# Kernel tuning notes

Hardware: AMD Instinct MI355X
Metric: run time of the kernel (lower is better)

The kernel has to match this reference:

```python
import jax, jax.numpy as jnp
import numpy as np

B, N, K, D, H = 16384, 10, 5, 512, 2
HD = D // H  # 256
IMG = 512.0


def setup_inputs() -> dict:
    key = jax.random.key(0)
    ks = jax.random.split(key, 18)
    w = lambda k, shape: (jax.random.normal(k, shape) * 0.02).astype(jnp.float32)
    boxes = jax.random.uniform(ks[0], (B, N, 4), minval=0.0, maxval=IMG, dtype=jnp.float32)
    return {
        'boxes': boxes,
        'w_in': w(ks[1], (D, K * 4)), 'b_in': jnp.zeros((D,), jnp.float32),
        'wqkv': w(ks[2], (3 * D, D)), 'bqkv': jnp.zeros((3 * D,), jnp.float32),
        'wo': w(ks[3], (D, D)), 'bo': jnp.zeros((D,), jnp.float32),
        'ln1_w': jnp.ones((D,), jnp.float32), 'ln1_b': jnp.zeros((D,), jnp.float32),
        'w1': w(ks[4], (D, D)), 'b1': jnp.zeros((D,), jnp.float32),
        'w2': w(ks[5], (D, D)), 'b2': jnp.zeros((D,), jnp.float32),
        'ln2_w': jnp.ones((D,), jnp.float32), 'ln2_b': jnp.zeros((D,), jnp.float32),
        'lnf_w': jnp.ones((D,), jnp.float32), 'lnf_b': jnp.zeros((D,), jnp.float32),
    }


def _ln(x, w, b, eps=1e-5):
    mu = jnp.mean(x, -1, keepdims=True)
    var = jnp.mean((x - mu) ** 2, -1, keepdims=True)
    return (x - mu) * jax.lax.rsqrt(var + eps) * w + b


def _relationships(boxes):
    # boxes: [B, N, 4] -> rel: [B, N, K*4]
    cx = (boxes[..., 0] + boxes[..., 2]) * 0.5 / IMG
    cy = (boxes[..., 1] + boxes[..., 3]) * 0.5 / IMG
    bw = jnp.abs(boxes[..., 2] - boxes[..., 0]) / IMG
    bh = jnp.abs(boxes[..., 3] - boxes[..., 1]) / IMG
    feats = jnp.stack([cx, cy, bw, bh], -1)  # [B, N, 4]
    dx = cx[:, :, None] - cx[:, None, :]
    dy = cy[:, :, None] - cy[:, None, :]
    dists = dx * dx + dy * dy  # [B, N, N]
    dists = jnp.where(jnp.eye(N, dtype=bool), jnp.inf, dists)
    _, idx = jax.lax.top_k(-dists, K)  # K smallest, ascending -> [B, N, K]
    nbr = jnp.take_along_axis(jnp.broadcast_to(feats[:, None], (B, N, N, 4)), idx[:, :, :, None], axis=2)  # [B, N, K, 4]
    return (nbr - feats[:, :, None, :]).reshape(B, N, K * 4)


def reference(boxes, w_in, b_in, wqkv, bqkv, wo, bo, ln1_w, ln1_b, w1, b1, w2, b2, ln2_w, ln2_b, lnf_w, lnf_b):
    rel = _relationships(boxes)                      # [B, N, 20]
    x = rel @ w_in.T + b_in                          # [B, N, D]
    # --- self attention (post-norm TransformerEncoderLayer, eval mode: no dropout) ---
    qkv = x @ wqkv.T + bqkv
    q, k, v = jnp.split(qkv, 3, axis=-1)
    split_heads = lambda t: t.reshape(B, N, H, HD).transpose(0, 2, 1, 3)
    q, k, v = split_heads(q), split_heads(k), split_heads(v)
    scores = jnp.einsum('bhqd,bhkd->bhqk', q, k) / jnp.sqrt(jnp.float32(HD))
    att = jax.nn.softmax(scores, axis=-1)
    o = jnp.einsum('bhqk,bhkd->bhqd', att, v).transpose(0, 2, 1, 3).reshape(B, N, D)
    x = _ln(x + o @ wo.T + bo, ln1_w, ln1_b)
    # --- feed forward ---
    ff = jax.nn.gelu(x @ w1.T + b1, approximate=False) @ w2.T + b2
    x = _ln(x + ff, ln2_w, ln2_b)
    return _ln(x, lnf_w, lnf_b)
```

## Files before the change

kernel.cpp:

```cpp
#include <hip/hip_runtime.h>
#include <hip/hip_bf16.h>
#include <math.h>

#define B_   16384
#define NT   10
#define KNN  5
#define D_   512
#define MTOT (B_*NT)

typedef __bf16 bf;
typedef __bf16 bfrag8 __attribute__((ext_vector_type(8)));
typedef float  floatx4 __attribute__((ext_vector_type(4)));

__device__ __forceinline__ float tof(bf x) { return (float)x; }
__device__ __forceinline__ bf    tob(float x) { return (bf)x; }

#define GLD_LDS(g, l) __builtin_amdgcn_global_load_lds( \
    (const __attribute__((address_space(1))) void*)(g), \
    (__attribute__((address_space(3))) void*)(l), 16, 0, 0)

__global__ void prep_folds(const float* __restrict__ wqkv, const float* __restrict__ bqkv,
                           const float* __restrict__ wo,   const float* __restrict__ bo,
                           bf* __restrict__ At, bf* __restrict__ Ct,
                           float* __restrict__ wconst, float* __restrict__ uvec)
{
    int gid = blockIdx.x, tid = threadIdx.x;
    if (gid < 4096) {
        int idx = gid * 256 + tid;
        int mat = idx >> 18;
        int rem = idx & 262143;
        int row = rem >> 9, col = rem & 511;
        float acc = 0.f;
        if (mat < 2) {
            int h = mat;
            const float* wq = wqkv + (size_t)(h * 256) * 512;
            const float* wk = wqkv + (size_t)(512 + h * 256) * 512;
            for (int c = 0; c < 256; ++c)
                acc += wq[c * 512 + col] * wk[c * 512 + row];
            At[(size_t)h * 262144 + row * 512 + col] = tob(acc * 0.0625f);
        } else {
            int h = mat - 2;
            const float* wv = wqkv + (size_t)(1024 + h * 256) * 512;
            for (int e = 0; e < 256; ++e)
                acc += wv[e * 512 + col] * wo[row * 512 + h * 256 + e];
            Ct[(size_t)h * 262144 + row * 512 + col] = tob(acc);
        }
    } else {
        for (int d = tid; d < 512; d += 256) {
            float acc = bo[d];
            for (int e = 0; e < 512; ++e)
                acc += bqkv[1024 + e] * wo[d * 512 + e];
            wconst[d] = acc;
            for (int h = 0; h < 2; ++h) {
                float u = 0.f;
                for (int c = 0; c < 256; ++c)
                    u += wqkv[(size_t)(512 + h * 256 + c) * 512 + d] * bqkv[h * 256 + c];
                uvec[h * 512 + d] = u * 0.0625f;
            }
        }
    }
}

__global__ void cvt_w(const float* __restrict__ src, bf* __restrict__ dst)
{
    int i = blockIdx.x * 256 + threadIdx.x;
    float4 v = *(const float4*)(src + (size_t)i * 4);
    bf o[4] = { tob(v.x), tob(v.y), tob(v.z), tob(v.w) };
    *(unsigned long long*)(dst + (size_t)i * 4) = *(unsigned long long*)o;
}

__global__ void rel_kernel(const float* __restrict__ boxes, float* __restrict__ rel)
{
#pragma clang fp contract(off)
    int gid = blockIdx.x * blockDim.x + threadIdx.x;
    if (gid >= MTOT) return;
    int b = gid / NT, n = gid % NT;
    const float* bx = boxes + (size_t)b * NT * 4;
    float cx[NT], cy[NT], bw[NT], bh[NT];
#pragma unroll
    for (int j = 0; j < NT; ++j) {
        float x0 = bx[j * 4 + 0], y0 = bx[j * 4 + 1];
        float x1 = bx[j * 4 + 2], y1 = bx[j * 4 + 3];
        cx[j] = ((x0 + x1) * 0.5f) * (1.f / 512.f);
        cy[j] = ((y0 + y1) * 0.5f) * (1.f / 512.f);
        bw[j] = fabsf(x1 - x0) * (1.f / 512.f);
        bh[j] = fabsf(y1 - y0) * (1.f / 512.f);
    }
    float dist[NT];
#pragma unroll
    for (int j = 0; j < NT; ++j) {
        float dx = cx[n] - cx[j], dy = cy[n] - cy[j];
        float dxx = dx * dx, dyy = dy * dy;
        dist[j] = (j == n) ? __builtin_inff() : (dxx + dyy);
    }
    float ocx = cx[n], ocy = cy[n], obw = bw[n], obh = bh[n];
#pragma unroll
    for (int k = 0; k < KNN; ++k) {
        int best = 0; float bd = __builtin_inff();
#pragma unroll
        for (int j = 0; j < NT; ++j)
            if (dist[j] < bd) { bd = dist[j]; best = j; }
        float fx = 0, fy = 0, fw = 0, fh = 0;
#pragma unroll
        for (int j = 0; j < NT; ++j)
            if (j == best) { fx = cx[j]; fy = cy[j]; fw = bw[j]; fh = bh[j]; dist[j] = __builtin_inff(); }
        size_t o = (size_t)gid * 20 + k * 4;
        rel[o + 0] = fx - ocx;
        rel[o + 1] = fy - ocy;
        rel[o + 2] = fw - obw;
        rel[o + 3] = fh - obh;
    }
}

__global__ void gemm_in(const float* __restrict__ rel, const float* __restrict__ w_in,
                        const float* __restrict__ b_in, bf* __restrict__ x0)
{
    __shared__ float relS[128][20];
    int tid = threadIdx.x;
    size_t tok0 = (size_t)blockIdx.x * 128;
    for (int i = tid; i < 128 * 20; i += 256)
        relS[i / 20][i % 20] = rel[tok0 * 20 + i];
    float w0[20], w1r[20];
#pragma unroll
    for (int j = 0; j < 20; ++j) {
        w0[j]  = w_in[tid * 20 + j];
        w1r[j] = w_in[(tid + 256) * 20 + j];
    }
    float bias0 = b_in[tid], bias1 = b_in[tid + 256];
    __syncthreads();
    for (int tk = 0; tk < 128; ++tk) {
        float a0 = bias0, a1 = bias1;
#pragma unroll
        for (int j = 0; j < 20; ++j) {
            float r = relS[tk][j];
            a0 += r * w0[j];
            a1 += r * w1r[j];
        }
        x0[(tok0 + tk) * 512 + tid]       = tob(a0);
        x0[(tok0 + tk) * 512 + tid + 256] = tob(a1);
    }
}

template <int EPI>
__launch_bounds__(512, 2)
__global__ void gemm_fn(const bf* __restrict__ A, const bf* __restrict__ Bt,
                        bf* __restrict__ out, const float* __restrict__ biasf)
{
    __shared__ bf As[2][128 * 32];
    __shared__ bf Bs[2][512 * 32];
    int tid = threadIdx.x;
    int w = tid >> 6, l = tid & 63;
    int lq = l >> 4, lr = l & 15;
    size_t m0 = (size_t)blockIdx.x * 128;
    int wm = (w & 1) * 64, wn = (w >> 1) * 128;
    floatx4 acc[4][8] = {};

    const bf* Ag = A + (m0 + (tid & 127)) * 512 + (tid >> 7) * 8;
    const bf* Bg = Bt + (size_t)tid * 512;

    auto stage = [&](int buf, int kt) {
        GLD_LDS(Ag + kt * 32, &As[buf][w * 512]);
#pragma unroll
        for (int p = 0; p < 4; ++p)
            GLD_LDS(Bg + kt * 32 + p * 8, &Bs[buf][(p * 512 + w * 64) * 8]);
    };

    stage(0, 0);
    asm volatile("s_waitcnt vmcnt(0)" ::: "memory");
    __builtin_amdgcn_s_barrier();
    __builtin_amdgcn_sched_barrier(0);

#pragma unroll 2
    for (int kt = 0; kt < 16; ++kt) {
        int cur = kt & 1;
        if (kt < 15) stage(cur ^ 1, kt + 1);

        const bf* as = &As[cur][(lq * 128 + wm + lr) * 8];
        const bf* bs = &Bs[cur][(lq * 512 + wn + lr) * 8];
        bfrag8 af[4], bfv[8];
#pragma unroll
        for (int i = 0; i < 4; ++i)
            af[i] = *(const bfrag8*)(as + i * 16 * 8);
#pragma unroll
        for (int j = 0; j < 8; ++j)
            bfv[j] = *(const bfrag8*)(bs + j * 16 * 8);
#pragma unroll
        for (int i = 0; i < 4; ++i)
#pragma unroll
            for (int j = 0; j < 8; ++j)
                acc[i][j] = __builtin_amdgcn_mfma_f32_16x16x32_bf16(af[i], bfv[j], acc[i][j], 0, 0, 0);

        if (kt < 15) {
            asm volatile("s_waitcnt vmcnt(0) lgkmcnt(0)" ::: "memory");
            __builtin_amdgcn_s_barrier();
            __builtin_amdgcn_sched_barrier(0);
        }
    }

#pragma unroll
    for (int i = 0; i < 4; ++i)
#pragma unroll
        for (int j = 0; j < 8; ++j) {
            int col = wn + j * 16 + lr;
#pragma unroll
            for (int r = 0; r < 4; ++r) {
                int row = wm + i * 16 + lq * 4 + r;
                float v = acc[i][j][r];
                if (EPI == 1) { v += biasf[col]; v = 0.5f * v * (1.f + erff(v * 0.70710678118654752f)); }
                if (EPI == 2) v += biasf[col];
                if (EPI == 3) v += tof(out[(m0 + row) * 512 + col]);
                out[(m0 + row) * 512 + col] = tob(v);
            }
        }
}

__global__ void scores_kernel(const bf* __restrict__ t, const bf* __restrict__ x0,
                              const float* __restrict__ uvec_h, float* __restrict__ att)
{
    int tid = threadIdx.x;
    int w = tid >> 6, l = tid & 63;
    int lq = l >> 4, lr = l & 15;
    size_t b = (size_t)blockIdx.x * 4 + w;
    const bf* trow = t  + (b * NT + lr) * 512;
    const bf* xrow = x0 + (b * NT + lr) * 512;
    floatx4 acc = {0.f, 0.f, 0.f, 0.f};
    float xu = 0.f;
#pragma unroll
    for (int kk = 0; kk < 16; ++kk) {
        bfrag8 a  = *(const bfrag8*)(trow + kk * 32 + lq * 8);
        bfrag8 bb = *(const bfrag8*)(xrow + kk * 32 + lq * 8);
        acc = __builtin_amdgcn_mfma_f32_16x16x32_bf16(a, bb, acc, 0, 0, 0);
#pragma unroll
        for (int jj = 0; jj < 8; ++jj)
            xu += (float)bb[jj] * uvec_h[kk * 32 + lq * 8 + jj];
    }
    xu += __shfl_xor(xu, 16);
    xu += __shfl_xor(xu, 32);
    bool jvalid = (lr < NT);
    float* ab = att + b * 100;
#pragma unroll
    for (int r = 0; r < 4; ++r) {
        float v = jvalid ? (acc[r] + xu) : -__builtin_inff();
        float m = v;
        m = fmaxf(m, __shfl_xor(m, 1)); m = fmaxf(m, __shfl_xor(m, 2));
        m = fmaxf(m, __shfl_xor(m, 4)); m = fmaxf(m, __shfl_xor(m, 8));
        float e = jvalid ? __expf(v - m) : 0.f;
        float s = e;
        s += __shfl_xor(s, 1); s += __shfl_xor(s, 2);
        s += __shfl_xor(s, 4); s += __shfl_xor(s, 8);
        float a = e / s;
        int i = lq * 4 + r;
        if (jvalid && i < NT) ab[i * 10 + lr] = a;
    }
}

__global__ void zmix(const float* __restrict__ att, const bf* __restrict__ x0, bf* __restrict__ z)
{
    __shared__ float xs[NT][512];
    __shared__ float as[100];
    size_t b = blockIdx.x;
    int tid = threadIdx.x;
    const bf* xb = x0 + b * NT * 512;
    for (int i = tid; i < NT * 512; i += 256) xs[i >> 9][i & 511] = tof(xb[i]);
    for (int i = tid; i < 100; i += 256) as[i] = att[b * 100 + i];
    __syncthreads();
    bf* zb = z + b * NT * 512;
    for (int o = tid; o < NT * 512; o += 256) {
        int i = o >> 9, d = o & 511;
        float a = 0.f;
#pragma unroll
        for (int j = 0; j < NT; ++j) a += as[i * 10 + j] * xs[j][d];
        zb[o] = tob(a);
    }
}

__global__ void ln_kernel(const bf* __restrict__ xin, const bf* __restrict__ yin,
                          const float* __restrict__ w, const float* __restrict__ bias,
                          bf* __restrict__ xout)
{
    int tid = threadIdx.x;
    int wv = tid >> 6, l = tid & 63;
    size_t tok = (size_t)blockIdx.x * 4 + wv;
    bfrag8 xv = *(const bfrag8*)(xin + tok * 512 + l * 8);
    bfrag8 yv = *(const bfrag8*)(yin + tok * 512 + l * 8);
    float v[8]; float s = 0.f;
#pragma unroll
    for (int i = 0; i < 8; ++i) { v[i] = (float)xv[i] + (float)yv[i]; s += v[i]; }
#pragma unroll
    for (int m = 1; m < 64; m <<= 1) s += __shfl_xor(s, m);
    float mu = s * (1.f / 512.f);
    float vs = 0.f;
#pragma unroll
    for (int i = 0; i < 8; ++i) { float d = v[i] - mu; vs += d * d; }
#pragma unroll
    for (int m = 1; m < 64; m <<= 1) vs += __shfl_xor(vs, m);
    float r = rsqrtf(vs * (1.f / 512.f) + 1e-5f);
    bfrag8 ov;
#pragma unroll
    for (int i = 0; i < 8; ++i) {
        int d = l * 8 + i;
        ov[i] = tob((v[i] - mu) * r * w[d] + bias[d]);
    }
    *(bfrag8*)(xout + tok * 512 + l * 8) = ov;
}

__global__ void final_kernel(const bf* __restrict__ x1, const bf* __restrict__ ff2,
                             const float* __restrict__ w2, const float* __restrict__ b2,
                             const float* __restrict__ wf, const float* __restrict__ bfi,
                             float* __restrict__ out)
{
    int tid = threadIdx.x;
    int wv = tid >> 6, l = tid & 63;
    size_t tok = (size_t)blockIdx.x * 4 + wv;
    bfrag8 xv = *(const bfrag8*)(x1 + tok * 512 + l * 8);
    bfrag8 yv = *(const bfrag8*)(ff2 + tok * 512 + l * 8);
    float v[8]; float s = 0.f;
#pragma unroll
    for (int i = 0; i < 8; ++i) { v[i] = (float)xv[i] + (float)yv[i]; s += v[i]; }
#pragma unroll
    for (int m = 1; m < 64; m <<= 1) s += __shfl_xor(s, m);
    float mu = s * (1.f / 512.f);
    float vs = 0.f;
#pragma unroll
    for (int i = 0; i < 8; ++i) { float d = v[i] - mu; vs += d * d; }
#pragma unroll
    for (int m = 1; m < 64; m <<= 1) vs += __shfl_xor(vs, m);
    float r = rsqrtf(vs * (1.f / 512.f) + 1e-5f);
    float u[8]; float s2 = 0.f;
#pragma unroll
    for (int i = 0; i < 8; ++i) {
        int d = l * 8 + i;
        u[i] = (v[i] - mu) * r * w2[d] + b2[d];
        s2 += u[i];
    }
#pragma unroll
    for (int m = 1; m < 64; m <<= 1) s2 += __shfl_xor(s2, m);
    float mu2 = s2 * (1.f / 512.f);
    float vs2 = 0.f;
#pragma unroll
    for (int i = 0; i < 8; ++i) { float d = u[i] - mu2; vs2 += d * d; }
#pragma unroll
    for (int m = 1; m < 64; m <<= 1) vs2 += __shfl_xor(vs2, m);
    float r2 = rsqrtf(vs2 * (1.f / 512.f) + 1e-5f);
    float4 o0, o1;
    float* op = (float*)&o0;
#pragma unroll
    for (int i = 0; i < 4; ++i) op[i] = (u[i] - mu2) * r2 * wf[l * 8 + i] + bfi[l * 8 + i];
    op = (float*)&o1;
#pragma unroll
    for (int i = 0; i < 4; ++i) op[i] = (u[4 + i] - mu2) * r2 * wf[l * 8 + 4 + i] + bfi[l * 8 + 4 + i];
    *(float4*)(out + tok * 512 + l * 8) = o0;
    *(float4*)(out + tok * 512 + l * 8 + 4) = o1;
}

extern "C" void kernel_launch(void* const* d_in, const int* in_sizes, int n_in,
                              void* d_out, int out_size, void* d_ws, size_t ws_size,
                              hipStream_t stream)
{
    const float* boxes = (const float*)d_in[0];
    const float* w_in  = (const float*)d_in[1];
    const float* b_in  = (const float*)d_in[2];
    const float* wqkv  = (const float*)d_in[3];
    const float* bqkv  = (const float*)d_in[4];
    const float* wo    = (const float*)d_in[5];
    const float* bo    = (const float*)d_in[6];
    const float* ln1w  = (const float*)d_in[7];
    const float* ln1b  = (const float*)d_in[8];
    const float* w1    = (const float*)d_in[9];
    const float* b1    = (const float*)d_in[10];
    const float* w2    = (const float*)d_in[11];
    const float* b2    = (const float*)d_in[12];
    const float* ln2w  = (const float*)d_in[13];
    const float* ln2b  = (const float*)d_in[14];
    const float* lnfw  = (const float*)d_in[15];
    const float* lnfb  = (const float*)d_in[16];
    float* out = (float*)d_out;

    char* ws = (char*)d_ws;
    bf*    At     = (bf*)(ws + 0);
    bf*    Ct     = (bf*)(ws + 1048576);
    bf*    W1b    = (bf*)(ws + 2097152);
    bf*    W2b    = (bf*)(ws + 2621440);
    float* wconst = (float*)(ws + 3145728);
    float* uvec   = (float*)(ws + 3147776);
    float* att    = (float*)(ws + 3151872);
    bf*    x0     = (bf*)(ws + 16259072);
    bf*    t      = (bf*)(ws + 184047616);
    bf*    y      = (bf*)(ws + 351836160);
    float* rel    = (float*)(ws + 184047616);

    dim3 gblk(256);
    dim3 gfn(MTOT / 128);

    prep_folds<<<4097, gblk, 0, stream>>>(wqkv, bqkv, wo, bo, At, Ct, wconst, uvec);
    cvt_w<<<256, gblk, 0, stream>>>(w1, W1b);
    cvt_w<<<256, gblk, 0, stream>>>(w2, W2b);
    rel_kernel<<<(MTOT + 255) / 256, gblk, 0, stream>>>(boxes, rel);
    gemm_in<<<MTOT / 128, gblk, 0, stream>>>(rel, w_in, b_in, x0);

    gemm_fn<0><<<gfn, 512, 0, stream>>>(x0, At, t, nullptr);
    scores_kernel<<<B_ / 4, gblk, 0, stream>>>(t, x0, uvec, att);
    gemm_fn<0><<<gfn, 512, 0, stream>>>(x0, At + 262144, t, nullptr);
    scores_kernel<<<B_ / 4, gblk, 0, stream>>>(t, x0, uvec + 512, att + (size_t)B_ * 100);
    zmix<<<B_, gblk, 0, stream>>>(att, x0, t);
    gemm_fn<2><<<gfn, 512, 0, stream>>>(t, Ct, y, wconst);
    zmix<<<B_, gblk, 0, stream>>>(att + (size_t)B_ * 100, x0, t);
    gemm_fn<3><<<gfn, 512, 0, stream>>>(t, Ct + 262144, y, nullptr);
    ln_kernel<<<MTOT / 4, gblk, 0, stream>>>(x0, y, ln1w, ln1b, x0);
    gemm_fn<1><<<gfn, 512, 0, stream>>>(x0, W1b, t, b1);
    gemm_fn<2><<<gfn, 512, 0, stream>>>(t, W2b, y, b2);
    final_kernel<<<MTOT / 4, gblk, 0, stream>>>(x0, y, ln2w, ln2b, lnfw, lnfb, out);
}
```

Measured before the change: 2.375 ms.

## Fuse attention mixing into scores kernel and retile GEMMs to 128x256 blocks

Merges the softmax-scores kernel with the attention-weighted mixing (zmix), so attention weights stay in shared memory and no longer round-trip through a global att buffer. The launch order is reorganised per head so each fused scores kernel writes z directly into t before the output-projection GEMM. The GEMM is retiled from 128x512 to 128x256 blocks on a 2D grid with 4 blocks per CU, with the barrier and wait placement changed to allow more overlap. gemm_in also reads rel via float4 loads. The smaller tile doubles A-operand reloads and the scores kernel now re-reads x0.

```diff
diff --git a/kernel.cpp b/kernel.cpp
--- a/kernel.cpp
+++ b/kernel.cpp
@@ -115,7 +115,7 @@
 __global__ void gemm_in(const float* __restrict__ rel, const float* __restrict__ w_in,
                         const float* __restrict__ b_in, bf* __restrict__ x0)
 {
-    __shared__ float relS[128][20];
+    __shared__ __align__(16) float relS[128][20];
     int tid = threadIdx.x;
     size_t tok0 = (size_t)blockIdx.x * 128;
     for (int i = tid; i < 128 * 20; i += 256)
@@ -129,12 +129,15 @@
     float bias0 = b_in[tid], bias1 = b_in[tid + 256];
     __syncthreads();
     for (int tk = 0; tk < 128; ++tk) {
+        const float4* rp = (const float4*)relS[tk];
         float a0 = bias0, a1 = bias1;
 #pragma unroll
-        for (int j = 0; j < 20; ++j) {
-            float r = relS[tk][j];
-            a0 += r * w0[j];
-            a1 += r * w1r[j];
+        for (int v4 = 0; v4 < 5; ++v4) {
+            float4 rv = rp[v4];
+            a0 += rv.x * w0[v4 * 4 + 0] + rv.y * w0[v4 * 4 + 1]
+                + rv.z * w0[v4 * 4 + 2] + rv.w * w0[v4 * 4 + 3];
+            a1 += rv.x * w1r[v4 * 4 + 0] + rv.y * w1r[v4 * 4 + 1]
+                + rv.z * w1r[v4 * 4 + 2] + rv.w * w1r[v4 * 4 + 3];
         }
         x0[(tok0 + tk) * 512 + tid]       = tob(a0);
         x0[(tok0 + tk) * 512 + tid + 256] = tob(a1);
@@ -142,86 +145,88 @@
 }
 
 template <int EPI>
-__launch_bounds__(512, 2)
-__global__ void gemm_fn(const bf* __restrict__ A, const bf* __restrict__ Bt,
-                        bf* __restrict__ out, const float* __restrict__ biasf)
-{
-    __shared__ bf As[2][128 * 32];
-    __shared__ bf Bs[2][512 * 32];
+__launch_bounds__(512, 4)
+__global__ void gemm2(const bf* __restrict__ A, const bf* __restrict__ Bt,
+                      bf* __restrict__ out, const float* __restrict__ biasf)
+{
+    __shared__ __align__(16) bf As[2][4096];
+    __shared__ __align__(16) bf Bs[2][8192];
     int tid = threadIdx.x;
     int w = tid >> 6, l = tid & 63;
     int lq = l >> 4, lr = l & 15;
-    size_t m0 = (size_t)blockIdx.x * 128;
-    int wm = (w & 1) * 64, wn = (w >> 1) * 128;
-    floatx4 acc[4][8] = {};
-
-    const bf* Ag = A + (m0 + (tid & 127)) * 512 + (tid >> 7) * 8;
-    const bf* Bg = Bt + (size_t)tid * 512;
+    size_t m0 = (size_t)blockIdx.y * 128;
+    int n0 = blockIdx.x * 256;
+    int wm = (w & 1) * 64, wn = (w >> 1) * 64;
+    floatx4 acc[4][4] = {};
+
+    const bf* Ag = A + (m0 + (size_t)(tid & 127)) * 512 + (tid >> 7) * 8;
+    const bf* Bg = Bt + (size_t)(n0 + (tid & 255)) * 512 + (tid >> 8) * 8;
 
     auto stage = [&](int buf, int kt) {
-        GLD_LDS(Ag + kt * 32, &As[buf][w * 512]);
-#pragma unroll
-        for (int p = 0; p < 4; ++p)
-            GLD_LDS(Bg + kt * 32 + p * 8, &Bs[buf][(p * 512 + w * 64) * 8]);
+        GLD_LDS(Ag + kt * 32,      &As[buf][w * 512]);
+        GLD_LDS(Bg + kt * 32,      &Bs[buf][w * 512]);
+        GLD_LDS(Bg + kt * 32 + 16, &Bs[buf][4096 + w * 512]);
     };
 
     stage(0, 0);
-    asm volatile("s_waitcnt vmcnt(0)" ::: "memory");
-    __builtin_amdgcn_s_barrier();
-    __builtin_amdgcn_sched_barrier(0);
-
 #pragma unroll 2
     for (int kt = 0; kt < 16; ++kt) {
         int cur = kt & 1;
-        if (kt < 15) stage(cur ^ 1, kt + 1);
+        if (kt < 15) {
+            stage(cur ^ 1, kt + 1);
+            asm volatile("s_waitcnt vmcnt(3)" ::: "memory");
+        } else {
+            asm volatile("s_waitcnt vmcnt(0)" ::: "memory");
+        }
+        __builtin_amdgcn_sched_barrier(0);
+        __builtin_amdgcn_s_barrier();
+        __builtin_amdgcn_sched_barrier(0);
 
         const bf* as = &As[cur][(lq * 128 + wm + lr) * 8];
-        const bf* bs = &Bs[cur][(lq * 512 + wn + lr) * 8];
-        bfrag8 af[4], bfv[8];
+        const bf* bs = &Bs[cur][(lq * 256 + wn + lr) * 8];
+        bfrag8 af[4], bfv[4];
+#pragma unroll
+        for (int i = 0; i < 4; ++i) af[i] = *(const bfrag8*)(as + i * 128);
+#pragma unroll
+        for (int j = 0; j < 4; ++j) bfv[j] = *(const bfrag8*)(bs + j * 128);
 #pragma unroll
         for (int i = 0; i < 4; ++i)
-            af[i] = *(const bfrag8*)(as + i * 16 * 8);
-#pragma unroll
-        for (int j = 0; j < 8; ++j)
-            bfv[j] = *(const bfrag8*)(bs + j * 16 * 8);
-#pragma unroll
-        for (int i = 0; i < 4; ++i)
-#pragma unroll
-            for (int j = 0; j < 8; ++j)
+#pragma unroll
+            for (int j = 0; j < 4; ++j)
                 acc[i][j] = __builtin_amdgcn_mfma_f32_16x16x32_bf16(af[i], bfv[j], acc[i][j], 0, 0, 0);
 
         if (kt < 15) {
-            asm volatile("s_waitcnt vmcnt(0) lgkmcnt(0)" ::: "memory");
+            __builtin_amdgcn_sched_barrier(0);
             __builtin_amdgcn_s_barrier();
-            __builtin_amdgcn_sched_barrier(0);
         }
     }
 
 #pragma unroll
     for (int i = 0; i < 4; ++i)
 #pragma unroll
-        for (int j = 0; j < 8; ++j) {
-            int col = wn + j * 16 + lr;
+        for (int j = 0; j < 4; ++j) {
+            int col = n0 + wn + j * 16 + lr;
 #pragma unroll
             for (int r = 0; r < 4; ++r) {
-                int row = wm + i * 16 + lq * 4 + r;
+                size_t row = m0 + wm + i * 16 + lq * 4 + r;
                 float v = acc[i][j][r];
                 if (EPI == 1) { v += biasf[col]; v = 0.5f * v * (1.f + erff(v * 0.70710678118654752f)); }
                 if (EPI == 2) v += biasf[col];
-                if (EPI == 3) v += tof(out[(m0 + row) * 512 + col]);
-                out[(m0 + row) * 512 + col] = tob(v);
+                if (EPI == 3) v += tof(out[row * 512 + col]);
+                out[row * 512 + col] = tob(v);
             }
         }
 }
 
-__global__ void scores_kernel(const bf* __restrict__ t, const bf* __restrict__ x0,
-                              const float* __restrict__ uvec_h, float* __restrict__ att)
-{
+__global__ void scoresz(bf* __restrict__ t, const bf* __restrict__ x0,
+                        const float* __restrict__ uvec_h)
+{
+    __shared__ float as[4][256];
     int tid = threadIdx.x;
     int w = tid >> 6, l = tid & 63;
     int lq = l >> 4, lr = l & 15;
     size_t b = (size_t)blockIdx.x * 4 + w;
-    const bf* trow = t  + (b * NT + lr) * 512;
+    bf* trow = t + (b * NT + lr) * 512;
     const bf* xrow = x0 + (b * NT + lr) * 512;
     floatx4 acc = {0.f, 0.f, 0.f, 0.f};
     float xu = 0.f;
@@ -237,7 +242,6 @@
     xu += __shfl_xor(xu, 16);
     xu += __shfl_xor(xu, 32);
     bool jvalid = (lr < NT);
-    float* ab = att + b * 100;
 #pragma unroll
     for (int r = 0; r < 4; ++r) {
         float v = jvalid ? (acc[r] + xu) : -__builtin_inff();
@@ -249,28 +253,26 @@
         s += __shfl_xor(s, 1); s += __shfl_xor(s, 2);
         s += __shfl_xor(s, 4); s += __shfl_xor(s, 8);
         float a = e / s;
-        int i = lq * 4 + r;
-        if (jvalid && i < NT) ab[i * 10 + lr] = a;
-    }
-}
-
-__global__ void zmix(const float* __restrict__ att, const bf* __restrict__ x0, bf* __restrict__ z)
-{
-    __shared__ float xs[NT][512];
-    __shared__ float as[100];
-    size_t b = blockIdx.x;
-    int tid = threadIdx.x;
-    const bf* xb = x0 + b * NT * 512;
-    for (int i = tid; i < NT * 512; i += 256) xs[i >> 9][i & 511] = tof(xb[i]);
-    for (int i = tid; i < 100; i += 256) as[i] = att[b * 100 + i];
+        as[w][(lq * 4 + r) * 16 + lr] = a;
+    }
     __syncthreads();
-    bf* zb = z + b * NT * 512;
-    for (int o = tid; o < NT * 512; o += 256) {
-        int i = o >> 9, d = o & 511;
-        float a = 0.f;
-#pragma unroll
-        for (int j = 0; j < NT; ++j) a += as[i * 10 + j] * xs[j][d];
-        zb[o] = tob(a);
+    bfrag8 xj[NT];
+#pragma unroll
+    for (int j = 0; j < NT; ++j)
+        xj[j] = *(const bfrag8*)(x0 + (b * NT + j) * 512 + l * 8);
+#pragma unroll
+    for (int i = 0; i < NT; ++i) {
+        float z[8] = {};
+#pragma unroll
+        for (int j = 0; j < NT; ++j) {
+            float a = as[w][i * 16 + j];
+#pragma unroll
+            for (int q = 0; q < 8; ++q) z[q] += a * (float)xj[j][q];
+        }
+        bfrag8 zv;
+#pragma unroll
+        for (int q = 0; q < 8; ++q) zv[q] = tob(z[q]);
+        *(bfrag8*)(t + (b * NT + i) * 512 + l * 8) = zv;
     }
 }
 
@@ -383,14 +385,13 @@
     bf*    W2b    = (bf*)(ws + 2621440);
     float* wconst = (float*)(ws + 3145728);
     float* uvec   = (float*)(ws + 3147776);
-    float* att    = (float*)(ws + 3151872);
     bf*    x0     = (bf*)(ws + 16259072);
     bf*    t      = (bf*)(ws + 184047616);
     bf*    y      = (bf*)(ws + 351836160);
     float* rel    = (float*)(ws + 184047616);
 
     dim3 gblk(256);
-    dim3 gfn(MTOT / 128);
+    dim3 ggemm(2, MTOT / 128);
 
     prep_folds<<<4097, gblk, 0, stream>>>(wqkv, bqkv, wo, bo, At, Ct, wconst, uvec);
     cvt_w<<<256, gblk, 0, stream>>>(w1, W1b);
@@ -398,16 +399,14 @@
     rel_kernel<<<(MTOT + 255) / 256, gblk, 0, stream>>>(boxes, rel);
     gemm_in<<<MTOT / 128, gblk, 0, stream>>>(rel, w_in, b_in, x0);
 
-    gemm_fn<0><<<gfn, 512, 0, stream>>>(x0, At, t, nullptr);
-    scores_kernel<<<B_ / 4, gblk, 0, stream>>>(t, x0, uvec, att);
-    gemm_fn<0><<<gfn, 512, 0, stream>>>(x0, At + 262144, t, nullptr);
-    scores_kernel<<<B_ / 4, gblk, 0, stream>>>(t, x0, uvec + 512, att + (size_t)B_ * 100);
-    zmix<<<B_, gblk, 0, stream>>>(att, x0, t);
-    gemm_fn<2><<<gfn, 512, 0, stream>>>(t, Ct, y, wconst);
-    zmix<<<B_, gblk, 0, stream>>>(att + (size_t)B_ * 100, x0, t);
-    gemm_fn<3><<<gfn, 512, 0, stream>>>(t, Ct + 262144, y, nullptr);
+    gemm2<0><<<ggemm, 512, 0, stream>>>(x0, At, t, nullptr);
+    scoresz<<<B_ / 4, gblk, 0, stream>>>(t, x0, uvec);
+    gemm2<2><<<ggemm, 512, 0, stream>>>(t, Ct, y, wconst);
+    gemm2<0><<<ggemm, 512, 0, stream>>>(x0, At + 262144, t, nullptr);
+    scoresz<<<B_ / 4, gblk, 0, stream>>>(t, x0, uvec + 512);
+    gemm2<3><<<ggemm, 512, 0, stream>>>(t, Ct + 262144, y, nullptr);
     ln_kernel<<<MTOT / 4, gblk, 0, stream>>>(x0, y, ln1w, ln1b, x0);
-    gemm_fn<1><<<gfn, 512, 0, stream>>>(x0, W1b, t, b1);
-    gemm_fn<2><<<gfn, 512, 0, stream>>>(t, W2b, y, b2);
+    gemm2<1><<<ggemm, 512, 0, stream>>>(x0, W1b, t, b1);
+    gemm2<2><<<ggemm, 512, 0, stream>>>(t, W2b, y, b2);
     final_kernel<<<MTOT / 4, gblk, 0, stream>>>(x0, y, ln2w, ln2b, lnfw, lnfb, out);
 }
```

Result: faster. 2.172 ms (-8.5%).
